# Performance work log

Hardware: AMD Instinct MI355X
Metric: run time of the kernel (lower is better)

Reference implementation:

```python
import jax, jax.numpy as jnp
import numpy as np

L = 3000          # nodes per modality
M = 3             # modalities
N = L * M         # total nodes
E = 200000        # edges
D = 512           # hidden_dim
S = D // 4        # shared_dim = 128
EPS = 1e-12       # F.normalize eps


def _lrelu(x):
    return jax.nn.leaky_relu(x, negative_slope=0.01)


def _l2norm(x):
    n = jnp.linalg.norm(x, axis=-1, keepdims=True)
    return x / jnp.maximum(n, EPS)


def setup_inputs() -> dict:
    key = jax.random.key(0)
    ks = jax.random.split(key, 16)
    w = lambda k, shape: (jax.random.normal(k, shape, dtype=jnp.float32) * 0.02)
    inp = {
        "feat0": jax.random.normal(ks[0], (L, D), dtype=jnp.float32),
        "feat1": jax.random.normal(ks[1], (L, D), dtype=jnp.float32),
        "feat2": jax.random.normal(ks[2], (L, D), dtype=jnp.float32),
        "edge_index": jax.random.randint(ks[3], (2, E), 0, N, dtype=jnp.int64),
        # EdgeWeightGen params (torch Linear convention: weight is (out, in))
        "proj_w": w(ks[4], (S, D)),
        "mlp_w1": w(ks[5], (S, 2 * S)),
        "mlp_b1": jnp.zeros((S,), dtype=jnp.float32),
        "mlp_w2": w(ks[6], (1, S)),
        "mlp_b2": jnp.zeros((1,), dtype=jnp.float32),
        # CrossModalGraphLayer params, 2 layers
        "W1_0": w(ks[7], (D, D)),
        "W2_0": w(ks[8], (D, 2 * D)),
        "W1_1": w(ks[9], (D, D)),
        "W2_1": w(ks[10], (D, 2 * D)),
    }
    return inp


def reference(feat0, feat1, feat2, edge_index, proj_w, mlp_w1, mlp_b1,
              mlp_w2, mlp_b2, W1_0, W2_0, W1_1, W2_1):
    feature = jnp.concatenate([feat0, feat1, feat2], axis=0)  # (N, D)
    src, tgt = edge_index[0], edge_index[1]

    # EdgeWeightGen
    shared_src = _l2norm(feature[src] @ proj_w.T)   # (E, S)
    shared_tgt = _l2norm(feature[tgt] @ proj_w.T)   # (E, S)
    emb_cat = jnp.concatenate([shared_src, shared_tgt], axis=-1)  # (E, 2S)
    h = _lrelu(emb_cat @ mlp_w1.T + mlp_b1)
    edge_weight = jax.nn.sigmoid((h @ mlp_w2.T + mlp_b2)[:, 0])   # (E,)

    # build_adj_matrix: dense scatter-add (sparse_coo coalesce sums dups)
    adj = jnp.zeros((N, N), dtype=feature.dtype).at[src, tgt].add(edge_weight)
    row_sum = adj.sum(axis=1)
    d_inv_sqrt = jnp.where(row_sum > 0, row_sum ** -0.5, 0.0)
    # D^{-1/2} A D^{-1/2} as elementwise row/col scaling (same math as diag matmuls)
    gcn = d_inv_sqrt[:, None] * adj * d_inv_sqrt[None, :]

    # graph layers
    x = feature
    for W1, W2 in ((W1_0, W2_0), (W1_1, W2_1)):
        proj = x @ W1.T                 # (N, D)
        nb = gcn @ proj                 # (N, D)
        cat = jnp.concatenate([x + nb, x * nb], axis=-1)  # (N, 2D)
        x = _lrelu(cat @ W2.T)
    return x  # concatenated updated features; chunk(x, 3) recovers per-modal tuple
```

## Files before the change

kernel.cpp:

```cpp
#include <hip/hip_runtime.h>
#include <hip/hip_bf16.h>
#include <math.h>

#define NL 3000
#define NN 9000
#define NE 200000
#define DD 512
#define SS 128
#define MPAD 9088
#define MT   (MPAD/16)

typedef __attribute__((ext_vector_type(8))) short    bf16x8;
typedef __attribute__((ext_vector_type(8))) ushort   u16x8;
typedef __attribute__((ext_vector_type(4))) float    f32x4;

static __device__ __forceinline__ ushort f2bf(float f){
  unsigned u = __float_as_uint(f);
  return (ushort)((u + 0x7FFFu + ((u>>16)&1u)) >> 16);
}
static __device__ __forceinline__ float bf2f(ushort u){
  return __uint_as_float(((unsigned)u)<<16);
}

__global__ __launch_bounds__(256) void k_packall(const float* __restrict__ f0, const float* __restrict__ f1,
                        const float* __restrict__ f2, const float* __restrict__ pw,
                        const float* __restrict__ w1,
                        const float* __restrict__ W10, const float* __restrict__ W20,
                        const float* __restrict__ W11, const float* __restrict__ W21,
                        short* __restrict__ Ap1, short* __restrict__ BpF,
                        short* __restrict__ Bp10, short* __restrict__ Bp20,
                        short* __restrict__ Bp11, short* __restrict__ Bp21,
                        short* __restrict__ Bpab,
                        float* __restrict__ row_sum, int* __restrict__ cnt){
  int b = blockIdx.x;
  int lane = threadIdx.x & 63;
  if (b < 2272){
    int t = b*4 + (threadIdx.x>>6);
    int tm = t >> 4, tk = t & 15;
    int m = tm*16 + (lane&15);
    int k = tk*32 + (lane>>4)*8;
    float4 v0 = make_float4(0,0,0,0), v1 = v0;
    if (m < NN){
      const float* srow = (m < NL) ? f0 + (size_t)m*DD
                         : (m < 2*NL) ? f1 + (size_t)(m-NL)*DD
                         : f2 + (size_t)(m-2*NL)*DD;
      v0 = *(const float4*)(srow + k);
      v1 = *(const float4*)(srow + k + 4);
    }
    u16x8 r;
    r[0]=f2bf(v0.x); r[1]=f2bf(v0.y); r[2]=f2bf(v0.z); r[3]=f2bf(v0.w);
    r[4]=f2bf(v1.x); r[5]=f2bf(v1.y); r[6]=f2bf(v1.z); r[7]=f2bf(v1.w);
    *(u16x8*)(Ap1 + (size_t)t*512 + lane*8) = r;
  } else if (b < 3072){
    int t = (b-2272)*4 + (threadIdx.x>>6);
    const float* X; short* P; int K, ntk, lt;
    if (t < 128)      { X=pw;  P=BpF;  K=512;  ntk=16; lt=t; }
    else if (t < 640) { X=W10; P=Bp10; K=512;  ntk=16; lt=t-128; }
    else if (t < 1664){ X=W20; P=Bp20; K=1024; ntk=32; lt=t-640; }
    else if (t < 2176){ X=W11; P=Bp11; K=512;  ntk=16; lt=t-1664; }
    else              { X=W21; P=Bp21; K=1024; ntk=32; lt=t-2176; }
    int tm = lt/ntk, tk = lt - tm*ntk;
    int m = tm*16 + (lane&15);
    int k = tk*32 + (lane>>4)*8;
    float4 v0 = *(const float4*)(X + (size_t)m*K + k);
    float4 v1 = *(const float4*)(X + (size_t)m*K + k + 4);
    u16x8 r;
    r[0]=f2bf(v0.x); r[1]=f2bf(v0.y); r[2]=f2bf(v0.z); r[3]=f2bf(v0.w);
    r[4]=f2bf(v1.x); r[5]=f2bf(v1.y); r[6]=f2bf(v1.z); r[7]=f2bf(v1.w);
    *(u16x8*)(P + (size_t)lt*512 + lane*8) = r;
  } else if (b < 3088){
    int t = (b-3072)*4 + (threadIdx.x>>6);
    int tn = t >> 2, tk = t & 3;
    int n = tn*16 + (lane&15);
    int k = tk*32 + (lane>>4)*8;
    const float* sp = (n<128) ? (w1 + (size_t)n*256 + k) : (w1 + (size_t)(n-128)*256 + 128 + k);
    float4 v0 = *(const float4*)sp;
    float4 v1 = *(const float4*)(sp+4);
    u16x8 r;
    r[0]=f2bf(v0.x); r[1]=f2bf(v0.y); r[2]=f2bf(v0.z); r[3]=f2bf(v0.w);
    r[4]=f2bf(v1.x); r[5]=f2bf(v1.y); r[6]=f2bf(v1.z); r[7]=f2bf(v1.w);
    *(u16x8*)(Bpab + (size_t)t*512 + lane*8) = r;
  } else {
    int idx = (b-3088)*256 + threadIdx.x;
    for (int i=idx; i<NN; i+=4608){ row_sum[i]=0.f; cnt[i]=0; }
  }
}

__global__ __launch_bounds__(256) void k_pack(const float* __restrict__ X, short* __restrict__ P,
                                              int M, int K, int nTilesK){
  int t = blockIdx.x*4 + (threadIdx.x>>6);
  int lane = threadIdx.x & 63;
  int tm = t / nTilesK, tk = t - tm*nTilesK;
  int m = tm*16 + (lane&15);
  int k = tk*32 + (lane>>4)*8;
  float4 v0 = make_float4(0,0,0,0), v1 = v0;
  if (m < M){
    v0 = *(const float4*)(X + (size_t)m*K + k);
    v1 = *(const float4*)(X + (size_t)m*K + k + 4);
  }
  u16x8 r;
  r[0]=f2bf(v0.x); r[1]=f2bf(v0.y); r[2]=f2bf(v0.z); r[3]=f2bf(v0.w);
  r[4]=f2bf(v1.x); r[5]=f2bf(v1.y); r[6]=f2bf(v1.z); r[7]=f2bf(v1.w);
  *(u16x8*)(P + (size_t)t*512 + lane*8) = r;
}

template<int ACT, int OBF>
__global__ __launch_bounds__(256) void k_gmm(const short* __restrict__ Ap, const short* __restrict__ Bp,
                                             void* __restrict__ Cv, int M, int N, int K){
  int l = blockIdx.x;
  int rr = l & 7, tt = l >> 3;
  int q = tt % 9, x = tt / 9;
  int y = q*8 + rr;
  if (y >= 71) return;
  int lane = threadIdx.x & 63, wave = threadIdx.x >> 6;
  int ktiles = K >> 5;
  int bm = y*128 + wave*32;
  int bn = x*64;
  const bf16x8* a0 = (const bf16x8*)(Ap + ((size_t)((bm>>4)  ) * ktiles)*512 + lane*8);
  const bf16x8* a1 = (const bf16x8*)(Ap + ((size_t)((bm>>4)+1) * ktiles)*512 + lane*8);
  const bf16x8* b0 = (const bf16x8*)(Bp + ((size_t)((bn>>4)  ) * ktiles)*512 + lane*8);
  const bf16x8* b1 = (const bf16x8*)(Bp + ((size_t)((bn>>4)+1) * ktiles)*512 + lane*8);
  const bf16x8* b2 = (const bf16x8*)(Bp + ((size_t)((bn>>4)+2) * ktiles)*512 + lane*8);
  const bf16x8* b3 = (const bf16x8*)(Bp + ((size_t)((bn>>4)+3) * ktiles)*512 + lane*8);
  f32x4 acc[2][4];
  #pragma unroll
  for (int i=0;i<2;++i)
    #pragma unroll
    for (int j=0;j<4;++j) acc[i][j] = (f32x4){0.f,0.f,0.f,0.f};

  for (int kt=0; kt<ktiles; ++kt){
    int off = kt*64;
    bf16x8 A0 = a0[off], A1 = a1[off];
    bf16x8 B0 = b0[off], B1 = b1[off], B2 = b2[off], B3 = b3[off];
    acc[0][0] = __builtin_amdgcn_mfma_f32_16x16x32_bf16(A0, B0, acc[0][0], 0,0,0);
    acc[0][1] = __builtin_amdgcn_mfma_f32_16x16x32_bf16(A0, B1, acc[0][1], 0,0,0);
    acc[0][2] = __builtin_amdgcn_mfma_f32_16x16x32_bf16(A0, B2, acc[0][2], 0,0,0);
    acc[0][3] = __builtin_amdgcn_mfma_f32_16x16x32_bf16(A0, B3, acc[0][3], 0,0,0);
    acc[1][0] = __builtin_amdgcn_mfma_f32_16x16x32_bf16(A1, B0, acc[1][0], 0,0,0);
    acc[1][1] = __builtin_amdgcn_mfma_f32_16x16x32_bf16(A1, B1, acc[1][1], 0,0,0);
    acc[1][2] = __builtin_amdgcn_mfma_f32_16x16x32_bf16(A1, B2, acc[1][2], 0,0,0);
    acc[1][3] = __builtin_amdgcn_mfma_f32_16x16x32_bf16(A1, B3, acc[1][3], 0,0,0);
  }
  int colo = lane & 15;
  int rowo = (lane >> 4) * 4;
  #pragma unroll
  for (int mi=0; mi<2; ++mi){
    #pragma unroll
    for (int r=0; r<4; ++r){
      int row = bm + mi*16 + rowo + r;
      if (row < M){
        #pragma unroll
        for (int ni=0; ni<4; ++ni){
          float v = acc[mi][ni][r];
          if (ACT) v = v>0.f ? v : 0.01f*v;
          int cidx = bn + ni*16 + colo;
          if (OBF) ((ushort*)Cv)[(size_t)row*N + cidx] = f2bf(v);
          else     ((float*) Cv)[(size_t)row*N + cidx] = v;
        }
      }
    }
  }
}

__global__ __launch_bounds__(256) void k_l2n(const float* __restrict__ X, short* __restrict__ ShP){
  int lane = threadIdx.x & 63, wave = threadIdx.x >> 6;
  int m = blockIdx.x*4 + wave;
  float2 v = ((const float2*)(X + (size_t)m*SS))[lane];
  float ss = v.x*v.x + v.y*v.y;
  #pragma unroll
  for (int o=32;o>0;o>>=1) ss += __shfl_xor(ss, o);
  float inv = 1.f / fmaxf(sqrtf(ss), 1e-12f);
  int k = 2*lane;
  int tIdx = (m>>4)*4 + (k>>5);
  int pos  = ((m&15) + ((k>>3)&3)*16)*8 + (k&7);
  ushort2 r; r.x = f2bf(v.x*inv); r.y = f2bf(v.y*inv);
  *(ushort2*)(ShP + (size_t)tIdx*512 + pos) = r;
}

__global__ __launch_bounds__(256) void k_edge(const int* __restrict__ src, const int* __restrict__ tgt,
                      const ushort* __restrict__ AB,
                      const float* __restrict__ b1, const float* __restrict__ w2,
                      const float* __restrict__ b2p,
                      float* __restrict__ ew, float* __restrict__ row_sum, int* __restrict__ cnt){
  int lane = threadIdx.x & 63;
  int p = lane & 15, g = lane >> 4;
  int wid = blockIdx.x*(blockDim.x>>6) + (threadIdx.x>>6);
  int nw  = gridDim.x*(blockDim.x>>6);
  float4 b1a = ((const float4*)b1)[p*2], b1b = ((const float4*)b1)[p*2+1];
  float4 w2a = ((const float4*)w2)[p*2], w2b = ((const float4*)w2)[p*2+1];
  float bb[8] = {b1a.x,b1a.y,b1a.z,b1a.w,b1b.x,b1b.y,b1b.z,b1b.w};
  float ww[8] = {w2a.x,w2a.y,w2a.z,w2a.w,w2b.x,w2b.y,w2b.z,w2b.w};
  float b2 = b2p[0];
  for (int e = wid*4+g; e < NE; e += nw*4){
    int s = src[e], tg_ = tgt[e];
    u16x8 av = *(const u16x8*)(AB + (size_t)s*256 + p*8);
    u16x8 bv = *(const u16x8*)(AB + (size_t)tg_*256 + 128 + p*8);
    float acc = 0.f;
    #pragma unroll
    for (int i=0;i<8;++i){
      float h = bf2f(av[i]) + bf2f(bv[i]) + bb[i];
      h = h>0.f ? h : 0.01f*h;
      acc += h*ww[i];
    }
    acc += __shfl_xor(acc,1); acc += __shfl_xor(acc,2);
    acc += __shfl_xor(acc,4); acc += __shfl_xor(acc,8);
    if (p==0){
      float wgt = 1.f/(1.f+expf(-(acc+b2)));
      ew[e]=wgt;
      atomicAdd(&row_sum[s], wgt);
      atomicAdd(&cnt[s], 1);
    }
  }
}

__global__ __launch_bounds__(1024) void k_scan(const int* __restrict__ cnt, const float* __restrict__ row_sum,
                      int* __restrict__ row_ptr, float* __restrict__ dinv, int* __restrict__ fill){
  __shared__ int wsum[16];
  int t = threadIdx.x;
  int lane = t & 63, wid = t >> 6;
  const int CH = 9;
  int base = t*CH;
  int v[CH]; int s = 0;
  #pragma unroll
  for (int i=0;i<CH;++i){
    int idx = base+i;
    v[i] = (idx<NN) ? cnt[idx] : 0;
    s += v[i];
  }
  int ps = s;
  #pragma unroll
  for (int o=1;o<64;o<<=1){
    int x = __shfl_up(ps, o);
    if (lane >= o) ps += x;
  }
  if (lane==63) wsum[wid] = ps;
  __syncthreads();
  if (wid==0){
    int wv = (lane<16)? wsum[lane] : 0;
    #pragma unroll
    for (int o=1;o<16;o<<=1){
      int x = __shfl_up(wv, o);
      if (lane>=o) wv += x;
    }
    if (lane<16) wsum[lane]=wv;
  }
  __syncthreads();
  int prefix = (wid>0 ? wsum[wid-1] : 0) + (ps - s);
  #pragma unroll
  for (int i=0;i<CH;++i){
    int idx = base+i;
    if (idx<NN){
      row_ptr[idx] = prefix;
      float rs = row_sum[idx];
      dinv[idx] = rs>0.f ? (1.f/sqrtf(rs)) : 0.f;
      fill[idx] = 0;
      prefix += v[i];
    }
  }
  if (t==1023) row_ptr[NN] = wsum[15];
}

__global__ __launch_bounds__(256) void k_scatter(const int* __restrict__ src, const int* __restrict__ tgt,
                        const float* __restrict__ ew, const float* __restrict__ dinv,
                        const int* __restrict__ row_ptr, int* __restrict__ fill,
                        int* __restrict__ col, float* __restrict__ coef){
  int e = blockIdx.x*blockDim.x+threadIdx.x;
  if (e>=NE) return;
  int s=src[e], tg=tgt[e];
  int pos = atomicAdd(&fill[s],1);
  int idx = row_ptr[s]+pos;
  col[idx]=tg;
  coef[idx]=dinv[s]*ew[e]*dinv[tg];
}

template<int LAYER>
__global__ __launch_bounds__(128) void k_spmm_cat(const int* __restrict__ row_ptr, const int* __restrict__ col,
                     const float* __restrict__ coef, const ushort* __restrict__ proj,
                     const float* __restrict__ xf0, const float* __restrict__ xf1,
                     const float* __restrict__ xf2,
                     short* __restrict__ P){
  int m = blockIdx.x, t = threadIdx.x;
  int beg = row_ptr[m], end = row_ptr[m+1];
  float4 a0 = make_float4(0,0,0,0), a1 = a0, a2 = a0, a3 = a0;
  int j = beg;
  for (; j+4<=end; j+=4){
    int c0=col[j], c1=col[j+1], c2=col[j+2], c3=col[j+3];
    float w0=coef[j], w1=coef[j+1], w2_=coef[j+2], w3=coef[j+3];
    ushort4 p0 = ((const ushort4*)(proj + (size_t)c0*DD))[t];
    ushort4 p1 = ((const ushort4*)(proj + (size_t)c1*DD))[t];
    ushort4 p2 = ((const ushort4*)(proj + (size_t)c2*DD))[t];
    ushort4 p3 = ((const ushort4*)(proj + (size_t)c3*DD))[t];
    a0.x += w0*bf2f(p0.x); a0.y += w0*bf2f(p0.y); a0.z += w0*bf2f(p0.z); a0.w += w0*bf2f(p0.w);
    a1.x += w1*bf2f(p1.x); a1.y += w1*bf2f(p1.y); a1.z += w1*bf2f(p1.z); a1.w += w1*bf2f(p1.w);
    a2.x += w2_*bf2f(p2.x); a2.y += w2_*bf2f(p2.y); a2.z += w2_*bf2f(p2.z); a2.w += w2_*bf2f(p2.w);
    a3.x += w3*bf2f(p3.x); a3.y += w3*bf2f(p3.y); a3.z += w3*bf2f(p3.z); a3.w += w3*bf2f(p3.w);
  }
  for (; j<end; ++j){
    int c0=col[j]; float w0=coef[j];
    ushort4 p0 = ((const ushort4*)(proj + (size_t)c0*DD))[t];
    a0.x += w0*bf2f(p0.x); a0.y += w0*bf2f(p0.y); a0.z += w0*bf2f(p0.z); a0.w += w0*bf2f(p0.w);
  }
  a0.x += a1.x + a2.x + a3.x;
  a0.y += a1.y + a2.y + a3.y;
  a0.z += a1.z + a2.z + a3.z;
  a0.w += a1.w + a2.w + a3.w;
  const float* xrow;
  if (LAYER==0){
    xrow = (m < NL) ? xf0 + (size_t)m*DD
         : (m < 2*NL) ? xf1 + (size_t)(m-NL)*DD
         : xf2 + (size_t)(m-2*NL)*DD;
  } else {
    xrow = xf0 + (size_t)m*DD;
  }
  float4 xv = ((const float4*)xrow)[t];
  float ax = xv.x + a0.x, ay = xv.y + a0.y, az = xv.z + a0.z, aw = xv.w + a0.w;
  float mx = xv.x * a0.x, my = xv.y * a0.y, mz = xv.z * a0.z, mw = xv.w * a0.w;
  ushort4 ra, rm;
  ra.x=f2bf(ax); ra.y=f2bf(ay); ra.z=f2bf(az); ra.w=f2bf(aw);
  rm.x=f2bf(mx); rm.y=f2bf(my); rm.z=f2bf(mz); rm.w=f2bf(mw);
  size_t tileA = (size_t)((m>>4)*32 + (t>>3));
  int    off   = ((m&15) + ((t>>1)&3)*16)*8 + (t&1)*4;
  *(ushort4*)(P + tileA*512 + off)        = ra;
  *(ushort4*)(P + (tileA+16)*512 + off)   = rm;
}

extern "C" void kernel_launch(void* const* d_in, const int* in_sizes, int n_in,
                              void* d_out, int out_size, void* d_ws, size_t ws_size,
                              hipStream_t stream){
  const float* f0 = (const float*)d_in[0];
  const float* f1 = (const float*)d_in[1];
  const float* f2 = (const float*)d_in[2];
  const int*   ei = (const int*)d_in[3];
  const float* pw = (const float*)d_in[4];
  const float* w1 = (const float*)d_in[5];
  const float* b1 = (const float*)d_in[6];
  const float* w2 = (const float*)d_in[7];
  const float* b2 = (const float*)d_in[8];
  const float* W1_0 = (const float*)d_in[9];
  const float* W2_0 = (const float*)d_in[10];
  const float* W1_1 = (const float*)d_in[11];
  const float* W2_1 = (const float*)d_in[12];
  float* out = (float*)d_out;

  const int* src = ei;
  const int* tgt = ei + NE;

  char* base = (char*)d_ws;
  size_t o = 0;
  auto alloc = [&](size_t bytes)->char*{ char* p = base + o; o += (bytes + 1023) & ~size_t(1023); return p; };
  float* x1      = (float*)alloc((size_t)NN*DD*4);
  ushort* projbf = (ushort*)alloc((size_t)NN*DD*2);
  float* projS   = (float*)alloc((size_t)NN*SS*4);
  ushort* ABn    = (ushort*)alloc((size_t)NN*256*2);
  short* Apack1  = (short*)alloc((size_t)MT*16*1024);
  short* Apack2  = (short*)alloc((size_t)MT*32*1024);
  short* ShP     = (short*)alloc((size_t)MT*4*1024);
  short* BpF     = (short*)alloc((size_t)8*16*1024);
  short* Bpab    = (short*)alloc((size_t)16*4*1024);
  short* Bp10    = (short*)alloc((size_t)32*16*1024);
  short* Bp20    = (short*)alloc((size_t)32*32*1024);
  short* Bp11    = (short*)alloc((size_t)32*16*1024);
  short* Bp21    = (short*)alloc((size_t)32*32*1024);
  float* ew      = (float*)alloc(NE*4);
  float* coef    = (float*)alloc(NE*4);
  float* row_sum = (float*)alloc(NN*4);
  int*   cnt     = (int*)alloc(NN*4);
  float* dinv    = (float*)alloc(NN*4);
  int*   fill    = (int*)alloc(NN*4);
  int*   row_ptr = (int*)alloc((NN+1)*4);
  int*   col     = (int*)alloc(NE*4);

  k_packall<<<3106, 256, 0, stream>>>(f0,f1,f2,pw,w1,W1_0,W2_0,W1_1,W2_1,
                                      Apack1,BpF,Bp10,Bp20,Bp11,Bp21,Bpab,row_sum,cnt);

  k_gmm<0,0><<<2*72, 256, 0, stream>>>(Apack1, BpF, projS, NN, 128, 512);
  k_l2n<<<NN/4, 256, 0, stream>>>(projS, ShP);
  k_gmm<0,1><<<4*72, 256, 0, stream>>>(ShP, Bpab, ABn, NN, 256, 128);

  k_edge<<<2048, 256, 0, stream>>>(src,tgt,ABn,b1,w2,b2,ew,row_sum,cnt);
  k_scan<<<1, 1024, 0, stream>>>(cnt,row_sum,row_ptr,dinv,fill);
  k_scatter<<<(NE+255)/256, 256, 0, stream>>>(src,tgt,ew,dinv,row_ptr,fill,col,coef);

  k_gmm<0,1><<<8*72, 256, 0, stream>>>(Apack1, Bp10, projbf, NN, DD, DD);
  k_spmm_cat<0><<<NN, 128, 0, stream>>>(row_ptr, col, coef, projbf, f0, f1, f2, Apack2);
  k_gmm<1,0><<<8*72, 256, 0, stream>>>(Apack2, Bp20, x1, NN, DD, 2*DD);
  k_pack<<<MT*16/4, 256, 0, stream>>>(x1, Apack1, NN, DD, 16);
  k_gmm<0,1><<<8*72, 256, 0, stream>>>(Apack1, Bp11, projbf, NN, DD, DD);
  k_spmm_cat<1><<<NN, 128, 0, stream>>>(row_ptr, col, coef, projbf, x1, nullptr, nullptr, Apack2);
  k_gmm<1,0><<<8*72, 256, 0, stream>>>(Apack2, Bp21, out, NN, DD, 2*DD);
}
```

Baseline: 322.6 us.

## Precount degrees early, fuse CSR scatter into edge kernel, widen GEMM N tile

Edge-source degree counting moves into the pack kernel, and the prefix scan runs before the edge MLP. This lets the edge kernel write CSR col and weight entries directly, so the separate scatter kernel and the coef array are gone. The symmetric normalisation is now applied inside the SpMM, using rsqrt of row_sum for the neighbour and the row. The GEMM tile is widened from 64 to 128 output columns, which doubles register accumulators and halves grid size. In exchange, the SpMM does extra random row_sum gathers, and the larger accumulator set may lower occupancy.

```diff
diff --git a/kernel.cpp b/kernel.cpp
--- a/kernel.cpp
+++ b/kernel.cpp
@@ -27,6 +27,7 @@
                         const float* __restrict__ w1,
                         const float* __restrict__ W10, const float* __restrict__ W20,
                         const float* __restrict__ W11, const float* __restrict__ W21,
+                        const int* __restrict__ src,
                         short* __restrict__ Ap1, short* __restrict__ BpF,
                         short* __restrict__ Bp10, short* __restrict__ Bp20,
                         short* __restrict__ Bp11, short* __restrict__ Bp21,
@@ -82,7 +83,8 @@
     *(u16x8*)(Bpab + (size_t)t*512 + lane*8) = r;
   } else {
     int idx = (b-3088)*256 + threadIdx.x;
-    for (int i=idx; i<NN; i+=4608){ row_sum[i]=0.f; cnt[i]=0; }
+    for (int i=idx; i<NN; i+=8192) row_sum[i]=0.f;
+    for (int e=idx; e<NE; e+=8192) atomicAdd(&cnt[src[e]],1);
   }
 }
 
@@ -115,31 +117,30 @@
   int lane = threadIdx.x & 63, wave = threadIdx.x >> 6;
   int ktiles = K >> 5;
   int bm = y*128 + wave*32;
-  int bn = x*64;
+  int bn = x*128;
   const bf16x8* a0 = (const bf16x8*)(Ap + ((size_t)((bm>>4)  ) * ktiles)*512 + lane*8);
   const bf16x8* a1 = (const bf16x8*)(Ap + ((size_t)((bm>>4)+1) * ktiles)*512 + lane*8);
-  const bf16x8* b0 = (const bf16x8*)(Bp + ((size_t)((bn>>4)  ) * ktiles)*512 + lane*8);
-  const bf16x8* b1 = (const bf16x8*)(Bp + ((size_t)((bn>>4)+1) * ktiles)*512 + lane*8);
-  const bf16x8* b2 = (const bf16x8*)(Bp + ((size_t)((bn>>4)+2) * ktiles)*512 + lane*8);
-  const bf16x8* b3 = (const bf16x8*)(Bp + ((size_t)((bn>>4)+3) * ktiles)*512 + lane*8);
-  f32x4 acc[2][4];
+  const bf16x8* bp[8];
+  #pragma unroll
+  for (int i=0;i<8;++i)
+    bp[i] = (const bf16x8*)(Bp + ((size_t)((bn>>4)+i) * ktiles)*512 + lane*8);
+  f32x4 acc[2][8];
   #pragma unroll
   for (int i=0;i<2;++i)
     #pragma unroll
-    for (int j=0;j<4;++j) acc[i][j] = (f32x4){0.f,0.f,0.f,0.f};
+    for (int j=0;j<8;++j) acc[i][j] = (f32x4){0.f,0.f,0.f,0.f};
 
   for (int kt=0; kt<ktiles; ++kt){
     int off = kt*64;
     bf16x8 A0 = a0[off], A1 = a1[off];
-    bf16x8 B0 = b0[off], B1 = b1[off], B2 = b2[off], B3 = b3[off];
-    acc[0][0] = __builtin_amdgcn_mfma_f32_16x16x32_bf16(A0, B0, acc[0][0], 0,0,0);
-    acc[0][1] = __builtin_amdgcn_mfma_f32_16x16x32_bf16(A0, B1, acc[0][1], 0,0,0);
-    acc[0][2] = __builtin_amdgcn_mfma_f32_16x16x32_bf16(A0, B2, acc[0][2], 0,0,0);
-    acc[0][3] = __builtin_amdgcn_mfma_f32_16x16x32_bf16(A0, B3, acc[0][3], 0,0,0);
-    acc[1][0] = __builtin_amdgcn_mfma_f32_16x16x32_bf16(A1, B0, acc[1][0], 0,0,0);
-    acc[1][1] = __builtin_amdgcn_mfma_f32_16x16x32_bf16(A1, B1, acc[1][1], 0,0,0);
-    acc[1][2] = __builtin_amdgcn_mfma_f32_16x16x32_bf16(A1, B2, acc[1][2], 0,0,0);
-    acc[1][3] = __builtin_amdgcn_mfma_f32_16x16x32_bf16(A1, B3, acc[1][3], 0,0,0);
+    bf16x8 Bf[8];
+    #pragma unroll
+    for (int i=0;i<8;++i) Bf[i] = bp[i][off];
+    #pragma unroll
+    for (int i=0;i<8;++i){
+      acc[0][i] = __builtin_amdgcn_mfma_f32_16x16x32_bf16(A0, Bf[i], acc[0][i], 0,0,0);
+      acc[1][i] = __builtin_amdgcn_mfma_f32_16x16x32_bf16(A1, Bf[i], acc[1][i], 0,0,0);
+    }
   }
   int colo = lane & 15;
   int rowo = (lane >> 4) * 4;
@@ -150,7 +151,7 @@
       int row = bm + mi*16 + rowo + r;
       if (row < M){
         #pragma unroll
-        for (int ni=0; ni<4; ++ni){
+        for (int ni=0; ni<8; ++ni){
           float v = acc[mi][ni][r];
           if (ACT) v = v>0.f ? v : 0.01f*v;
           int cidx = bn + ni*16 + colo;
@@ -181,7 +182,9 @@
                       const ushort* __restrict__ AB,
                       const float* __restrict__ b1, const float* __restrict__ w2,
                       const float* __restrict__ b2p,
-                      float* __restrict__ ew, float* __restrict__ row_sum, int* __restrict__ cnt){
+                      const int* __restrict__ row_ptr, int* __restrict__ fill,
+                      int* __restrict__ col, float* __restrict__ ewC,
+                      float* __restrict__ row_sum){
   int lane = threadIdx.x & 63;
   int p = lane & 15, g = lane >> 4;
   int wid = blockIdx.x*(blockDim.x>>6) + (threadIdx.x>>6);
@@ -206,15 +209,17 @@
     acc += __shfl_xor(acc,4); acc += __shfl_xor(acc,8);
     if (p==0){
       float wgt = 1.f/(1.f+expf(-(acc+b2)));
-      ew[e]=wgt;
+      int pos = atomicAdd(&fill[s],1);
+      int idx = row_ptr[s]+pos;
+      col[idx]=tg_;
+      ewC[idx]=wgt;
       atomicAdd(&row_sum[s], wgt);
-      atomicAdd(&cnt[s], 1);
-    }
-  }
-}
-
-__global__ __launch_bounds__(1024) void k_scan(const int* __restrict__ cnt, const float* __restrict__ row_sum,
-                      int* __restrict__ row_ptr, float* __restrict__ dinv, int* __restrict__ fill){
+    }
+  }
+}
+
+__global__ __launch_bounds__(1024) void k_scan(const int* __restrict__ cnt,
+                      int* __restrict__ row_ptr, int* __restrict__ fill){
   __shared__ int wsum[16];
   int t = threadIdx.x;
   int lane = t & 63, wid = t >> 6;
@@ -251,8 +256,6 @@
     int idx = base+i;
     if (idx<NN){
       row_ptr[idx] = prefix;
-      float rs = row_sum[idx];
-      dinv[idx] = rs>0.f ? (1.f/sqrtf(rs)) : 0.f;
       fill[idx] = 0;
       prefix += v[i];
     }
@@ -260,32 +263,26 @@
   if (t==1023) row_ptr[NN] = wsum[15];
 }
 
-__global__ __launch_bounds__(256) void k_scatter(const int* __restrict__ src, const int* __restrict__ tgt,
-                        const float* __restrict__ ew, const float* __restrict__ dinv,
-                        const int* __restrict__ row_ptr, int* __restrict__ fill,
-                        int* __restrict__ col, float* __restrict__ coef){
-  int e = blockIdx.x*blockDim.x+threadIdx.x;
-  if (e>=NE) return;
-  int s=src[e], tg=tgt[e];
-  int pos = atomicAdd(&fill[s],1);
-  int idx = row_ptr[s]+pos;
-  col[idx]=tg;
-  coef[idx]=dinv[s]*ew[e]*dinv[tg];
-}
-
 template<int LAYER>
 __global__ __launch_bounds__(128) void k_spmm_cat(const int* __restrict__ row_ptr, const int* __restrict__ col,
-                     const float* __restrict__ coef, const ushort* __restrict__ proj,
+                     const float* __restrict__ ew, const float* __restrict__ row_sum,
+                     const ushort* __restrict__ proj,
                      const float* __restrict__ xf0, const float* __restrict__ xf1,
                      const float* __restrict__ xf2,
                      short* __restrict__ P){
   int m = blockIdx.x, t = threadIdx.x;
   int beg = row_ptr[m], end = row_ptr[m+1];
+  float rsm = row_sum[m];
+  float dim = rsm>0.f ? rsqrtf(rsm) : 0.f;
   float4 a0 = make_float4(0,0,0,0), a1 = a0, a2 = a0, a3 = a0;
   int j = beg;
   for (; j+4<=end; j+=4){
     int c0=col[j], c1=col[j+1], c2=col[j+2], c3=col[j+3];
-    float w0=coef[j], w1=coef[j+1], w2_=coef[j+2], w3=coef[j+3];
+    float r0=row_sum[c0], r1=row_sum[c1], r2=row_sum[c2], r3=row_sum[c3];
+    float w0=ew[j]  *(r0>0.f?rsqrtf(r0):0.f);
+    float w1=ew[j+1]*(r1>0.f?rsqrtf(r1):0.f);
+    float w2_=ew[j+2]*(r2>0.f?rsqrtf(r2):0.f);
+    float w3=ew[j+3]*(r3>0.f?rsqrtf(r3):0.f);
     ushort4 p0 = ((const ushort4*)(proj + (size_t)c0*DD))[t];
     ushort4 p1 = ((const ushort4*)(proj + (size_t)c1*DD))[t];
     ushort4 p2 = ((const ushort4*)(proj + (size_t)c2*DD))[t];
@@ -296,14 +293,16 @@
     a3.x += w3*bf2f(p3.x); a3.y += w3*bf2f(p3.y); a3.z += w3*bf2f(p3.z); a3.w += w3*bf2f(p3.w);
   }
   for (; j<end; ++j){
-    int c0=col[j]; float w0=coef[j];
+    int c0=col[j];
+    float r0=row_sum[c0];
+    float w0=ew[j]*(r0>0.f?rsqrtf(r0):0.f);
     ushort4 p0 = ((const ushort4*)(proj + (size_t)c0*DD))[t];
     a0.x += w0*bf2f(p0.x); a0.y += w0*bf2f(p0.y); a0.z += w0*bf2f(p0.z); a0.w += w0*bf2f(p0.w);
   }
-  a0.x += a1.x + a2.x + a3.x;
-  a0.y += a1.y + a2.y + a3.y;
-  a0.z += a1.z + a2.z + a3.z;
-  a0.w += a1.w + a2.w + a3.w;
+  a0.x = dim*(a0.x + a1.x + a2.x + a3.x);
+  a0.y = dim*(a0.y + a1.y + a2.y + a3.y);
+  a0.z = dim*(a0.z + a1.z + a2.z + a3.z);
+  a0.w = dim*(a0.w + a1.w + a2.w + a3.w);
   const float* xrow;
   if (LAYER==0){
     xrow = (m < NL) ? xf0 + (size_t)m*DD
@@ -362,30 +361,29 @@
   short* Bp11    = (short*)alloc((size_t)32*16*1024);
   short* Bp21    = (short*)alloc((size_t)32*32*1024);
   float* ew      = (float*)alloc(NE*4);
-  float* coef    = (float*)alloc(NE*4);
   float* row_sum = (float*)alloc(NN*4);
   int*   cnt     = (int*)alloc(NN*4);
-  float* dinv    = (float*)alloc(NN*4);
   int*   fill    = (int*)alloc(NN*4);
   int*   row_ptr = (int*)alloc((NN+1)*4);
   int*   col     = (int*)alloc(NE*4);
 
-  k_packall<<<3106, 256, 0, stream>>>(f0,f1,f2,pw,w1,W1_0,W2_0,W1_1,W2_1,
+  hipMemsetAsync(cnt, 0, NN*4, stream);
+
+  k_packall<<<3120, 256, 0, stream>>>(f0,f1,f2,pw,w1,W1_0,W2_0,W1_1,W2_1,src,
                                       Apack1,BpF,Bp10,Bp20,Bp11,Bp21,Bpab,row_sum,cnt);
-
-  k_gmm<0,0><<<2*72, 256, 0, stream>>>(Apack1, BpF, projS, NN, 128, 512);
+  k_scan<<<1, 1024, 0, stream>>>(cnt,row_ptr,fill);
+
+  k_gmm<0,0><<<1*72, 256, 0, stream>>>(Apack1, BpF, projS, NN, 128, 512);
   k_l2n<<<NN/4, 256, 0, stream>>>(projS, ShP);
-  k_gmm<0,1><<<4*72, 256, 0, stream>>>(ShP, Bpab, ABn, NN, 256, 128);
-
-  k_edge<<<2048, 256, 0, stream>>>(src,tgt,ABn,b1,w2,b2,ew,row_sum,cnt);
-  k_scan<<<1, 1024, 0, stream>>>(cnt,row_sum,row_ptr,dinv,fill);
-  k_scatter<<<(NE+255)/256, 256, 0, stream>>>(src,tgt,ew,dinv,row_ptr,fill,col,coef);
-
-  k_gmm<0,1><<<8*72, 256, 0, stream>>>(Apack1, Bp10, projbf, NN, DD, DD);
-  k_spmm_cat<0><<<NN, 128, 0, stream>>>(row_ptr, col, coef, projbf, f0, f1, f2, Apack2);
-  k_gmm<1,0><<<8*72, 256, 0, stream>>>(Apack2, Bp20, x1, NN, DD, 2*DD);
+  k_gmm<0,1><<<2*72, 256, 0, stream>>>(ShP, Bpab, ABn, NN, 256, 128);
+
+  k_edge<<<2048, 256, 0, stream>>>(src,tgt,ABn,b1,w2,b2,row_ptr,fill,col,ew,row_sum);
+
+  k_gmm<0,1><<<4*72, 256, 0, stream>>>(Apack1, Bp10, projbf, NN, DD, DD);
+  k_spmm_cat<0><<<NN, 128, 0, stream>>>(row_ptr, col, ew, row_sum, projbf, f0, f1, f2, Apack2);
+  k_gmm<1,0><<<4*72, 256, 0, stream>>>(Apack2, Bp20, x1, NN, DD, 2*DD);
   k_pack<<<MT*16/4, 256, 0, stream>>>(x1, Apack1, NN, DD, 16);
-  k_gmm<0,1><<<8*72, 256, 0, stream>>>(Apack1, Bp11, projbf, NN, DD, DD);
-  k_spmm_cat<1><<<NN, 128, 0, stream>>>(row_ptr, col, coef, projbf, x1, nullptr, nullptr, Apack2);
-  k_gmm<1,0><<<8*72, 256, 0, stream>>>(Apack2, Bp21, out, NN, DD, 2*DD);
-}
+  k_gmm<0,1><<<4*72, 256, 0, stream>>>(Apack1, Bp11, projbf, NN, DD, DD);
+  k_spmm_cat<1><<<NN, 128, 0, stream>>>(row_ptr, col, ew, row_sum, projbf, x1, nullptr, nullptr, Apack2);
+  k_gmm<1,0><<<4*72, 256, 0, stream>>>(Apack2, Bp21, out, NN, DD, 2*DD);
+}
```

Result: no change. 326.9 us (+1.3%).
